# Kernel optimization log

Hardware: AMD Instinct MI355X
Metric: run time of the kernel (lower is better)

Reference implementation:

```python
import jax, jax.numpy as jnp
import numpy as np

TOPK = 2          # activate_experts
N_EXPERTS = 8     # n_routed_experts
ROUTER_SCALE = 1.0
EPS = 1e-20


def setup_inputs() -> dict:
    key = jax.random.key(0)
    ks = jax.random.split(key, 9)
    B, S, D, H, E = 4, 1024, 2048, 1792, N_EXPERTS
    w_std = 0.02  # realistic init scale so sigmoid gate is not saturated
    return {
        "x": jax.random.normal(ks[0], (B, S, D), jnp.float32),
        "gate_w": jax.random.normal(ks[1], (E, D), jnp.float32) * w_std,
        "w1_shared": jax.random.normal(ks[2], (H, D), jnp.float32) * w_std,
        "w2_shared": jax.random.normal(ks[3], (D, H), jnp.float32) * w_std,
        "w3_shared": jax.random.normal(ks[4], (H, D), jnp.float32) * w_std,
        "w1_experts": jax.random.normal(ks[5], (E, H, D), jnp.float32) * w_std,
        "w2_experts": jax.random.normal(ks[6], (E, D, H), jnp.float32) * w_std,
        "w3_experts": jax.random.normal(ks[7], (E, H, D), jnp.float32) * w_std,
        "expert_bias": jnp.zeros((E,), jnp.float32),
    }


def _swiglu(x, w1, w2, w3):
    # FeedForward.forward: w2(silu(w1(x)) * w3(x)), no biases, Identity norm
    return (jax.nn.silu(x @ w1.T) * (x @ w3.T)) @ w2.T


def reference(x, gate_w, w1_shared, w2_shared, w3_shared,
              w1_experts, w2_experts, w3_experts, expert_bias):
    B, S, D = x.shape
    xf = x.reshape(B * S, D)
    N = B * S

    # shared expert path
    out = _swiglu(xf, w1_shared, w2_shared, w3_shared)

    # ---- TokenChoiceTopKRouter ----
    scores = jax.nn.sigmoid((xf @ gate_w.T).astype(jnp.float32))      # [N, E]
    _, idx = jax.lax.top_k(scores + expert_bias[None, :], TOPK)       # [N, K]
    top = jnp.take_along_axis(scores, idx, axis=1)                    # [N, K]
    top = top / (jnp.sum(top, axis=-1, keepdims=True) + EPS)

    # dense gate matrix g[t,e] = normalized score if expert e selected for token t, else 0.
    # Equivalent to the permute -> grouped-GEMM -> scatter_add pipeline: the
    # scaling (top_scores * router_scaling_factor) is applied to the expert
    # INPUT, and since the expert FFN has no biases, FFN_e(0) == 0 for
    # unselected experts, so the scatter_add combine equals a sum over e.
    g = jnp.zeros((N, N_EXPERTS), scores.dtype)
    g = g.at[jnp.arange(N)[:, None], idx].set(top) * ROUTER_SCALE      # [N, E]

    xg = xf[:, None, :] * g[:, :, None]                                # [N, E, D]
    h = jax.nn.silu(jnp.einsum('ned,ehd->neh', xg, w1_experts)) \
        * jnp.einsum('ned,ehd->neh', xg, w3_experts)                   # [N, E, H]
    out = out + jnp.einsum('neh,edh->nd', h, w2_experts)               # combine over experts

    output = out.reshape(B, S, D)
    aux_loss = jnp.float32(0.0)  # eval mode: aux_loss = 0
    return output, aux_loss
```

## Files before the change

kernel.cpp:

```cpp
#include <hip/hip_runtime.h>
#include <stdint.h>

typedef unsigned short u16;
typedef short v8s __attribute__((ext_vector_type(8)));
typedef float v4f __attribute__((ext_vector_type(4)));

#define NTOK 4096
#define DDIM 2048
#define HDIM 1792
#define NEXP 8
#define MAXROWS 9216
#define MAXTILE 72

__device__ __forceinline__ u16 f2b(float f) {
    union { float f; uint32_t i; } v; v.f = f;
    uint32_t r = v.i + 0x7fff + ((v.i >> 16) & 1);
    return (u16)(r >> 16);
}
__device__ __forceinline__ float silu_f(float x) { return x / (1.f + __expf(-x)); }
__device__ __forceinline__ float b2f(u16 u) {
    union { float f; uint32_t i; } v; v.i = ((uint32_t)u) << 16; return v.f;
}

#define AS1 __attribute__((address_space(1)))
#define AS3 __attribute__((address_space(3)))
__device__ __forceinline__ void gload_lds16(const u16* g, u16* l) {
    __builtin_amdgcn_global_load_lds((const AS1 void*)g, (AS3 void*)l, 16, 0, 0);
}

__global__ void cvt_kernel(const float* __restrict__ in, u16* __restrict__ out, int n) {
    int i = (blockIdx.x * blockDim.x + threadIdx.x) * 4;
    if (i >= n) return;
    float4 v = *(const float4*)(in + i);
    ushort4 o;
    o.x = f2b(v.x); o.y = f2b(v.y); o.z = f2b(v.z); o.w = f2b(v.w);
    *(ushort4*)(out + i) = o;
}

__global__ void router_kernel(const float* __restrict__ x, const float* __restrict__ gw,
                              const float* __restrict__ bias,
                              int* __restrict__ topk_idx, float* __restrict__ topk_wt,
                              int* __restrict__ cnt) {
    int wave = threadIdx.x >> 6, lane = threadIdx.x & 63;
    int t = blockIdx.x * 4 + wave;
    float acc[NEXP];
#pragma unroll
    for (int e = 0; e < NEXP; e++) acc[e] = 0.f;
    const float* xr = x + (size_t)t * DDIM;
    for (int i = 0; i < DDIM / 64; i++) {
        int d = i * 64 + lane;
        float xv = xr[d];
#pragma unroll
        for (int e = 0; e < NEXP; e++) acc[e] += xv * gw[e * DDIM + d];
    }
#pragma unroll
    for (int off = 32; off > 0; off >>= 1)
#pragma unroll
        for (int e = 0; e < NEXP; e++) acc[e] += __shfl_xor(acc[e], off, 64);
    if (lane == 0) {
        float s[NEXP], sb[NEXP];
#pragma unroll
        for (int e = 0; e < NEXP; e++) {
            s[e] = 1.f / (1.f + __expf(-acc[e]));
            sb[e] = s[e] + bias[e];
        }
        int i0 = 0;
#pragma unroll
        for (int e = 1; e < NEXP; e++) if (sb[e] > sb[i0]) i0 = e;
        int i1 = -1;
#pragma unroll
        for (int e = 0; e < NEXP; e++) {
            if (e == i0) continue;
            if (i1 < 0 || sb[e] > sb[i1]) i1 = e;
        }
        float w0 = s[i0], w1 = s[i1];
        float inv = 1.f / (w0 + w1 + 1e-20f);
        topk_idx[t * 2] = i0; topk_idx[t * 2 + 1] = i1;
        topk_wt[t * 2] = w0 * inv; topk_wt[t * 2 + 1] = w1 * inv;
        atomicAdd(&cnt[i0], 1); atomicAdd(&cnt[i1], 1);
    }
}

__global__ void zero_small(int* cnt, int* cnt2) {
    if (threadIdx.x < NEXP) { cnt[threadIdx.x] = 0; cnt2[threadIdx.x] = 0; }
}

__global__ void setup_kernel(const int* __restrict__ cnt, int* __restrict__ base,
                             int* __restrict__ exp_tile, int* __restrict__ tok_of,
                             float* __restrict__ wt_of) {
    if (threadIdx.x == 0) {
        int b = 0, sb[NEXP + 1];
        for (int e = 0; e < NEXP; e++) { sb[e] = b; base[e] = b; b += (cnt[e] + 127) & ~127; }
        sb[NEXP] = b; base[NEXP] = b;
        int ntile = b >> 7;
        for (int td = 0; td < MAXTILE; td++) {
            int e = -1;
            if (td < ntile) {
                int r = td << 7;
                for (int q = 0; q < NEXP; q++)
                    if (r >= sb[q] && r < sb[q + 1]) e = q;
            }
            exp_tile[td] = e;
        }
    }
    __syncthreads();
    for (int i = threadIdx.x; i < MAXROWS; i += blockDim.x) { tok_of[i] = 0; wt_of[i] = 0.f; }
}

__global__ void assign_kernel(const int* __restrict__ topk_idx, const float* __restrict__ topk_wt,
                              const int* __restrict__ base, int* __restrict__ cnt2,
                              int* __restrict__ tok_of, float* __restrict__ wt_of) {
    int g = blockIdx.x * blockDim.x + threadIdx.x;
    int t = g >> 1, k = g & 1;
    int e = topk_idx[t * 2 + k];
    int p = base[e] + atomicAdd(&cnt2[e], 1);
    tok_of[p] = t; wt_of[p] = topk_wt[t * 2 + k];
}

template <int EPI, bool GATHER, bool EXPB, bool BF32>
__global__ __launch_bounds__(256, 2)
void gemm_nt(const u16* __restrict__ A, const void* __restrict__ Bw,
             void* __restrict__ Cout, int N, int K,
             const int* __restrict__ tok_of, const int* __restrict__ exp_tile,
             long bstride) {
    int nt = blockIdx.x, mt = blockIdx.y;
    size_t boff = 0;
    if (EXPB) {
        int e = exp_tile[mt];
        if (e < 0) return;
        boff = (size_t)e * bstride;
    }
    int m0 = mt * 128, n0 = nt * 128;
    __shared__ u16 As[128 * 64];
    __shared__ u16 Bs[128 * 64];
    int tid = threadIdx.x, lane = tid & 63, wave = tid >> 6;
    int wm = wave >> 1, wn = wave & 1;
    int quad = lane >> 4, lr = lane & 15;

    v4f acc[4][4];
#pragma unroll
    for (int i = 0; i < 4; i++)
#pragma unroll
        for (int j = 0; j < 4; j++) acc[i][j] = (v4f){0.f, 0.f, 0.f, 0.f};

    const u16* gA[4];
    const u16* gB[4];
    const float* fB[4];
    u16* sB[4];
    u16* lA[4];
    u16* lB[4];
#pragma unroll
    for (int j = 0; j < 4; j++) {
        int idx = j * 256 + tid;
        int row = idx >> 3, s = idx & 7, cc = s ^ (row & 7);
        int arow = GATHER ? tok_of[m0 + row] : (m0 + row);
        gA[j] = A + (size_t)arow * K + cc * 8;
        if (!BF32) {
            gB[j] = (const u16*)Bw + boff + (size_t)(n0 + row) * K + cc * 8;
            fB[j] = nullptr; sB[j] = nullptr;
        } else {
            gB[j] = nullptr;
            fB[j] = (const float*)Bw + boff + (size_t)(n0 + row) * K + cc * 8;
            sB[j] = Bs + (size_t)idx * 8;
        }
        int cb = (j * 256 + wave * 64) * 8;
        lA[j] = As + cb;
        lB[j] = Bs + cb;
    }

    for (int k0 = 0; k0 < K; k0 += 64) {
#pragma unroll
        for (int j = 0; j < 4; j++) gload_lds16(gA[j] + k0, lA[j]);
        if (!BF32) {
#pragma unroll
            for (int j = 0; j < 4; j++) gload_lds16(gB[j] + k0, lB[j]);
        } else {
#pragma unroll
            for (int j = 0; j < 4; j++) {
                const float* bp = fB[j] + k0;
                float4 f0 = *(const float4*)bp;
                float4 f1 = *(const float4*)(bp + 4);
                union { v8s v; u16 s[8]; } u;
                u.s[0] = f2b(f0.x); u.s[1] = f2b(f0.y); u.s[2] = f2b(f0.z); u.s[3] = f2b(f0.w);
                u.s[4] = f2b(f1.x); u.s[5] = f2b(f1.y); u.s[6] = f2b(f1.z); u.s[7] = f2b(f1.w);
                *(v8s*)sB[j] = u.v;
            }
        }
        __syncthreads();
#pragma unroll
        for (int kk = 0; kk < 64; kk += 32) {
            v8s af[4], bfr[4];
#pragma unroll
            for (int mi = 0; mi < 4; mi++) {
                int row = wm * 64 + mi * 16 + lr;
                int c = (kk >> 3) + quad;
                af[mi] = *(const v8s*)(As + row * 64 + ((c ^ (row & 7)) << 3));
            }
#pragma unroll
            for (int ni = 0; ni < 4; ni++) {
                int row = wn * 64 + ni * 16 + lr;
                int c = (kk >> 3) + quad;
                bfr[ni] = *(const v8s*)(Bs + row * 64 + ((c ^ (row & 7)) << 3));
            }
#pragma unroll
            for (int mi = 0; mi < 4; mi++)
#pragma unroll
                for (int ni = 0; ni < 4; ni++)
                    acc[mi][ni] = __builtin_amdgcn_mfma_f32_16x16x32_bf16(af[mi], bfr[ni], acc[mi][ni], 0, 0, 0);
        }
        __syncthreads();
    }

#pragma unroll
    for (int mi = 0; mi < 4; mi++)
#pragma unroll
        for (int ni = 0; ni < 4; ni++)
#pragma unroll
            for (int r = 0; r < 4; r++) {
                int gr = m0 + wm * 64 + mi * 16 + quad * 4 + r;
                int gc = n0 + wn * 64 + ni * 16 + lr;
                float v = acc[mi][ni][r];
                if (EPI == 0) {
                    ((u16*)Cout)[(size_t)gr * N + gc] = f2b(v);
                } else if (EPI == 1) {
                    ((float*)Cout)[(size_t)gr * N + gc] = v;
                } else {
                    int tok = tok_of[gr];
                    atomicAdd(&((float*)Cout)[(size_t)tok * N + gc], v);
                }
            }
}

__global__ void swiglu_kernel(u16* __restrict__ u1, const u16* __restrict__ u3,
                              const float* __restrict__ wt_of) {
    int row = blockIdx.x;
    float w = wt_of ? wt_of[row] : 1.f;
    size_t i = (size_t)row * HDIM + threadIdx.x * 4;
    ushort4 a = *(const ushort4*)(u1 + i);
    ushort4 b = *(const ushort4*)(u3 + i);
    ushort4 o;
    o.x = f2b(silu_f(w * b2f(a.x)) * (w * b2f(b.x)));
    o.y = f2b(silu_f(w * b2f(a.y)) * (w * b2f(b.y)));
    o.z = f2b(silu_f(w * b2f(a.z)) * (w * b2f(b.z)));
    o.w = f2b(silu_f(w * b2f(a.w)) * (w * b2f(b.w)));
    *(ushort4*)(u1 + i) = o;
}

__global__ void aux_kernel(float* __restrict__ out) {
    if (threadIdx.x == 0) out[(size_t)NTOK * DDIM] = 0.f;
}

extern "C" void kernel_launch(void* const* d_in, const int* in_sizes, int n_in,
                              void* d_out, int out_size, void* d_ws, size_t ws_size,
                              hipStream_t stream) {
    const float* x   = (const float*)d_in[0];
    const float* gw  = (const float*)d_in[1];
    const float* w1s = (const float*)d_in[2];
    const float* w2s = (const float*)d_in[3];
    const float* w3s = (const float*)d_in[4];
    const float* w1e = (const float*)d_in[5];
    const float* w2e = (const float*)d_in[6];
    const float* w3e = (const float*)d_in[7];
    const float* ebias = (const float*)d_in[8];
    float* outp = (float*)d_out;

    char* ws = (char*)d_ws;
    size_t off = 0;
    auto alloc = [&](size_t bytes) {
        void* p = ws + off;
        off = (off + bytes + 255) & ~(size_t)255;
        return p;
    };
    u16* xb     = (u16*)alloc((size_t)NTOK * DDIM * 2);
    u16* u1     = (u16*)alloc((size_t)MAXROWS * HDIM * 2);
    u16* u3     = (u16*)alloc((size_t)MAXROWS * HDIM * 2);
    int* topk_idx = (int*)alloc(NTOK * 2 * 4);
    float* topk_wt = (float*)alloc(NTOK * 2 * 4);
    int* cnt    = (int*)alloc(64);
    int* cnt2   = (int*)alloc(64);
    int* base   = (int*)alloc(64);
    int* exp_tile = (int*)alloc(MAXTILE * 4);
    int* tok_of = (int*)alloc(MAXROWS * 4);
    float* wt_of = (float*)alloc(MAXROWS * 4);
    const int SH = HDIM * DDIM;
    const long EX = (long)NEXP * HDIM * DDIM;
    u16* w1sb = (u16*)alloc((size_t)SH * 2);
    u16* w2sb = (u16*)alloc((size_t)SH * 2);
    u16* w3sb = (u16*)alloc((size_t)SH * 2);
    u16* w1eb = (u16*)alloc((size_t)EX * 2);
    u16* w2eb = (u16*)alloc((size_t)EX * 2);
    u16* w3eb = (u16*)alloc((size_t)EX * 2);
    bool full = (off <= ws_size);
    (void)in_sizes; (void)n_in; (void)out_size;

    zero_small<<<1, 64, 0, stream>>>(cnt, cnt2);
    router_kernel<<<NTOK / 4, 256, 0, stream>>>(x, gw, ebias, topk_idx, topk_wt, cnt);
    setup_kernel<<<1, 256, 0, stream>>>(cnt, base, exp_tile, tok_of, wt_of);
    assign_kernel<<<NTOK * 2 / 256, 256, 0, stream>>>(topk_idx, topk_wt, base, cnt2, tok_of, wt_of);

    cvt_kernel<<<(NTOK * DDIM / 4 + 255) / 256, 256, 0, stream>>>(x, xb, NTOK * DDIM);
    if (full) {
        cvt_kernel<<<(SH / 4 + 255) / 256, 256, 0, stream>>>(w1s, w1sb, SH);
        cvt_kernel<<<(SH / 4 + 255) / 256, 256, 0, stream>>>(w2s, w2sb, SH);
        cvt_kernel<<<(SH / 4 + 255) / 256, 256, 0, stream>>>(w3s, w3sb, SH);
        cvt_kernel<<<((int)(EX / 4) + 255) / 256, 256, 0, stream>>>(w1e, w1eb, (int)EX);
        cvt_kernel<<<((int)(EX / 4) + 255) / 256, 256, 0, stream>>>(w2e, w2eb, (int)EX);
        cvt_kernel<<<((int)(EX / 4) + 255) / 256, 256, 0, stream>>>(w3e, w3eb, (int)EX);
    }

    if (full) {
        gemm_nt<0, false, false, false><<<dim3(HDIM / 128, NTOK / 128), 256, 0, stream>>>(
            xb, w1sb, u1, HDIM, DDIM, nullptr, nullptr, 0);
        gemm_nt<0, false, false, false><<<dim3(HDIM / 128, NTOK / 128), 256, 0, stream>>>(
            xb, w3sb, u3, HDIM, DDIM, nullptr, nullptr, 0);
        swiglu_kernel<<<NTOK, 448, 0, stream>>>(u1, u3, nullptr);
        gemm_nt<1, false, false, false><<<dim3(DDIM / 128, NTOK / 128), 256, 0, stream>>>(
            u1, w2sb, outp, DDIM, HDIM, nullptr, nullptr, 0);
        gemm_nt<0, true, true, false><<<dim3(HDIM / 128, MAXTILE), 256, 0, stream>>>(
            xb, w1eb, u1, HDIM, DDIM, tok_of, exp_tile, (long)HDIM * DDIM);
        gemm_nt<0, true, true, false><<<dim3(HDIM / 128, MAXTILE), 256, 0, stream>>>(
            xb, w3eb, u3, HDIM, DDIM, tok_of, exp_tile, (long)HDIM * DDIM);
        swiglu_kernel<<<MAXROWS, 448, 0, stream>>>(u1, u3, wt_of);
        gemm_nt<2, false, true, false><<<dim3(DDIM / 128, MAXTILE), 256, 0, stream>>>(
            u1, w2eb, outp, DDIM, HDIM, tok_of, exp_tile, (long)DDIM * HDIM);
    } else {
        gemm_nt<0, false, false, true><<<dim3(HDIM / 128, NTOK / 128), 256, 0, stream>>>(
            xb, w1s, u1, HDIM, DDIM, nullptr, nullptr, 0);
        gemm_nt<0, false, false, true><<<dim3(HDIM / 128, NTOK / 128), 256, 0, stream>>>(
            xb, w3s, u3, HDIM, DDIM, nullptr, nullptr, 0);
        swiglu_kernel<<<NTOK, 448, 0, stream>>>(u1, u3, nullptr);
        gemm_nt<1, false, false, true><<<dim3(DDIM / 128, NTOK / 128), 256, 0, stream>>>(
            u1, w2s, outp, DDIM, HDIM, nullptr, nullptr, 0);
        gemm_nt<0, true, true, true><<<dim3(HDIM / 128, MAXTILE), 256, 0, stream>>>(
            xb, w1e, u1, HDIM, DDIM, tok_of, exp_tile, (long)HDIM * DDIM);
        gemm_nt<0, true, true, true><<<dim3(HDIM / 128, MAXTILE), 256, 0, stream>>>(
            xb, w3e, u3, HDIM, DDIM, tok_of, exp_tile, (long)HDIM * DDIM);
        swiglu_kernel<<<MAXROWS, 448, 0, stream>>>(u1, u3, wt_of);
        gemm_nt<2, false, true, true><<<dim3(DDIM / 128, MAXTILE), 256, 0, stream>>>(
            u1, w2e, outp, DDIM, HDIM, tok_of, exp_tile, (long)DDIM * HDIM);
    }

    aux_kernel<<<1, 64, 0, stream>>>(outp);
}
```

Measured before the change: 1.021 ms.

## Fold shared expert into grouped GEMM with 256x256 multi-stage pipelined tiles

The shared expert is treated as a ninth expert occupying the first 4096 rows of the grouped buffer, which removes the separate shared-path GEMM launches. The bf16 GEMM is replaced with a 256x256-tile, 512-thread kernel that keeps a 4-stage LDS ring filled by async global-to-LDS loads, uses explicit vmcnt waits and raises wave priority around the MFMA block. Per-expert padding grows to 256 rows, so more padded rows are computed. The shared output now goes through atomic adds into a zeroed output buffer, which adds a memset and extra atomic traffic.

New measurement: 1.153 ms. +13.0%, slower.

```diff
diff --git a/kernel.cpp b/kernel.cpp
--- a/kernel.cpp
+++ b/kernel.cpp
@@ -9,8 +9,10 @@
 #define DDIM 2048
 #define HDIM 1792
 #define NEXP 8
-#define MAXROWS 9216
-#define MAXTILE 72
+#define SHROWS 4096
+#define MAXROWS 14336
+#define MAXT256 56
+#define MAXT128 112
 
 __device__ __forceinline__ u16 f2b(float f) {
     union { float f; uint32_t i; } v; v.f = f;
@@ -27,6 +29,7 @@
 __device__ __forceinline__ void gload_lds16(const u16* g, u16* l) {
     __builtin_amdgcn_global_load_lds((const AS1 void*)g, (AS3 void*)l, 16, 0, 0);
 }
+#define WAITV(n) asm volatile("s_waitcnt vmcnt(" #n ")" ::: "memory")
 
 __global__ void cvt_kernel(const float* __restrict__ in, u16* __restrict__ out, int n) {
     int i = (blockIdx.x * blockDim.x + threadIdx.x) * 4;
@@ -86,25 +89,32 @@
 }
 
 __global__ void setup_kernel(const int* __restrict__ cnt, int* __restrict__ base,
-                             int* __restrict__ exp_tile, int* __restrict__ tok_of,
-                             float* __restrict__ wt_of) {
+                             int* __restrict__ exp_tile256, int* __restrict__ exp_tile128,
+                             int* __restrict__ tok_of, float* __restrict__ wt_of) {
     if (threadIdx.x == 0) {
-        int b = 0, sb[NEXP + 1];
-        for (int e = 0; e < NEXP; e++) { sb[e] = b; base[e] = b; b += (cnt[e] + 127) & ~127; }
-        sb[NEXP] = b; base[NEXP] = b;
-        int ntile = b >> 7;
-        for (int td = 0; td < MAXTILE; td++) {
-            int e = -1;
-            if (td < ntile) {
-                int r = td << 7;
-                for (int q = 0; q < NEXP; q++)
-                    if (r >= sb[q] && r < sb[q + 1]) e = q;
-            }
-            exp_tile[td] = e;
+        int b = SHROWS, sb[NEXP + 1];
+        for (int e = 0; e < NEXP; e++) { sb[e] = b; base[e] = b; b += (cnt[e] + 255) & ~255; }
+        sb[NEXP] = b;
+        for (int td = 0; td < MAXT256; td++) {
+            int e = -1, r = td << 8;
+            if (r < SHROWS) e = NEXP;
+            else for (int q = 0; q < NEXP; q++)
+                if (r >= sb[q] && r < sb[q + 1]) e = q;
+            exp_tile256[td] = e;
+        }
+        for (int td = 0; td < MAXT128; td++) {
+            int e = -1, r = td << 7;
+            if (r < SHROWS) e = NEXP;
+            else for (int q = 0; q < NEXP; q++)
+                if (r >= sb[q] && r < sb[q + 1]) e = q;
+            exp_tile128[td] = e;
         }
     }
     __syncthreads();
-    for (int i = threadIdx.x; i < MAXROWS; i += blockDim.x) { tok_of[i] = 0; wt_of[i] = 0.f; }
+    for (int i = threadIdx.x; i < MAXROWS; i += blockDim.x) {
+        tok_of[i] = (i < SHROWS) ? i : 0;
+        wt_of[i]  = (i < SHROWS) ? 1.f : 0.f;
+    }
 }
 
 __global__ void assign_kernel(const int* __restrict__ topk_idx, const float* __restrict__ topk_wt,
@@ -117,19 +127,121 @@
     tok_of[p] = t; wt_of[p] = topk_wt[t * 2 + k];
 }
 
-template <int EPI, bool GATHER, bool EXPB, bool BF32>
-__global__ __launch_bounds__(256, 2)
-void gemm_nt(const u16* __restrict__ A, const void* __restrict__ Bw,
-             void* __restrict__ Cout, int N, int K,
+template <int EPI, bool GATHER, int K>
+__global__ __launch_bounds__(512, 2)
+void gemm256(const u16* __restrict__ A, const u16* __restrict__ Bw,
+             void* __restrict__ Cout, int N,
              const int* __restrict__ tok_of, const int* __restrict__ exp_tile,
              long bstride) {
+    constexpr int NT = K / 32;
     int nt = blockIdx.x, mt = blockIdx.y;
-    size_t boff = 0;
-    if (EXPB) {
-        int e = exp_tile[mt];
-        if (e < 0) return;
-        boff = (size_t)e * bstride;
-    }
+    int e = exp_tile[mt];
+    if (e < 0) return;
+    const u16* Bp = Bw + (size_t)e * bstride;
+    int m0 = mt * 256, n0 = nt * 256;
+
+    __shared__ u16 smem[4 * 2 * 8192];
+    int tid = threadIdx.x, lane = tid & 63, wave = tid >> 6;
+    int wm = wave >> 2, wn = wave & 3, quad = lane >> 4, lr = lane & 15;
+
+    v4f acc[8][4];
+#pragma unroll
+    for (int i = 0; i < 8; i++)
+#pragma unroll
+        for (int j = 0; j < 4; j++) acc[i][j] = (v4f){0.f, 0.f, 0.f, 0.f};
+
+    const u16* gA[2]; const u16* gB[2]; int ldso[2];
+#pragma unroll
+    for (int j = 0; j < 2; j++) {
+        int idx = j * 512 + tid;
+        int R = idx >> 3, s = idx & 7, cc = s ^ (R & 7);
+        int r = (R << 1) | (cc >> 2);
+        int col = (cc & 3) * 8;
+        int ar = GATHER ? tok_of[m0 + r] : (m0 + r);
+        gA[j] = A + (size_t)ar * K + col;
+        gB[j] = Bp + (size_t)(n0 + r) * K + col;
+        ldso[j] = (j * 512 + wave * 64) * 8;
+    }
+    int offA[8], offB[4];
+#pragma unroll
+    for (int mi = 0; mi < 8; mi++) {
+        int r = wm * 128 + mi * 16 + lr;
+        int R = r >> 1, cc = ((r & 1) << 2) | quad;
+        offA[mi] = R * 64 + ((cc ^ (R & 7)) << 3);
+    }
+#pragma unroll
+    for (int ni = 0; ni < 4; ni++) {
+        int r = wn * 64 + ni * 16 + lr;
+        int R = r >> 1, cc = ((r & 1) << 2) | quad;
+        offB[ni] = R * 64 + ((cc ^ (R & 7)) << 3);
+    }
+
+    auto STAGE = [&](int t) {
+        u16* base = smem + (t & 3) * 16384;
+        int k0 = t * 32;
+#pragma unroll
+        for (int j = 0; j < 2; j++) gload_lds16(gA[j] + k0, base + ldso[j]);
+#pragma unroll
+        for (int j = 0; j < 2; j++) gload_lds16(gB[j] + k0, base + 8192 + ldso[j]);
+    };
+
+    STAGE(0); STAGE(1); STAGE(2);
+
+#pragma unroll 1
+    for (int t = 0; t < NT; t++) {
+        if (t + 3 < NT) STAGE(t + 3);
+        if      (t + 3 < NT) { WAITV(12); }
+        else if (t + 2 < NT) { WAITV(8); }
+        else if (t + 1 < NT) { WAITV(4); }
+        else                 { WAITV(0); }
+        __builtin_amdgcn_s_barrier();
+        const u16* sa = smem + (t & 3) * 16384;
+        const u16* sb = sa + 8192;
+        v8s af[8], bfr[4];
+#pragma unroll
+        for (int mi = 0; mi < 8; mi++) af[mi] = *(const v8s*)(sa + offA[mi]);
+#pragma unroll
+        for (int ni = 0; ni < 4; ni++) bfr[ni] = *(const v8s*)(sb + offB[ni]);
+        asm volatile("s_waitcnt lgkmcnt(0)" ::: "memory");
+        __builtin_amdgcn_sched_barrier(0);
+        __builtin_amdgcn_s_setprio(1);
+#pragma unroll
+        for (int mi = 0; mi < 8; mi++)
+#pragma unroll
+            for (int ni = 0; ni < 4; ni++)
+                acc[mi][ni] = __builtin_amdgcn_mfma_f32_16x16x32_bf16(af[mi], bfr[ni], acc[mi][ni], 0, 0, 0);
+        __builtin_amdgcn_s_setprio(0);
+        __builtin_amdgcn_s_barrier();
+    }
+
+#pragma unroll
+    for (int mi = 0; mi < 8; mi++)
+#pragma unroll
+        for (int ni = 0; ni < 4; ni++)
+#pragma unroll
+            for (int r = 0; r < 4; r++) {
+                int gr = m0 + wm * 128 + mi * 16 + quad * 4 + r;
+                int gc = n0 + wn * 64 + ni * 16 + lr;
+                float v = acc[mi][ni][r];
+                if (EPI == 0) {
+                    ((u16*)Cout)[(size_t)gr * N + gc] = f2b(v);
+                } else {
+                    int tok = tok_of[gr];
+                    atomicAdd(&((float*)Cout)[(size_t)tok * N + gc], v);
+                }
+            }
+}
+
+template <int EPI, bool GATHER>
+__global__ __launch_bounds__(256, 2)
+void gemm_nt_f32(const u16* __restrict__ A, const float* __restrict__ Bw,
+                 const float* __restrict__ Bsh, void* __restrict__ Cout, int N, int K,
+                 const int* __restrict__ tok_of, const int* __restrict__ exp_tile,
+                 long bstride) {
+    int nt = blockIdx.x, mt = blockIdx.y;
+    int e = exp_tile[mt];
+    if (e < 0) return;
+    const float* Bp = (e == NEXP) ? Bsh : (Bw + (size_t)e * bstride);
     int m0 = mt * 128, n0 = nt * 128;
     __shared__ u16 As[128 * 64];
     __shared__ u16 Bs[128 * 64];
@@ -143,48 +255,30 @@
 #pragma unroll
         for (int j = 0; j < 4; j++) acc[i][j] = (v4f){0.f, 0.f, 0.f, 0.f};
 
-    const u16* gA[4];
-    const u16* gB[4];
-    const float* fB[4];
-    u16* sB[4];
-    u16* lA[4];
-    u16* lB[4];
+    const u16* gA[4]; const float* fB[4]; u16* sB[4]; u16* lA[4];
 #pragma unroll
     for (int j = 0; j < 4; j++) {
         int idx = j * 256 + tid;
         int row = idx >> 3, s = idx & 7, cc = s ^ (row & 7);
         int arow = GATHER ? tok_of[m0 + row] : (m0 + row);
         gA[j] = A + (size_t)arow * K + cc * 8;
-        if (!BF32) {
-            gB[j] = (const u16*)Bw + boff + (size_t)(n0 + row) * K + cc * 8;
-            fB[j] = nullptr; sB[j] = nullptr;
-        } else {
-            gB[j] = nullptr;
-            fB[j] = (const float*)Bw + boff + (size_t)(n0 + row) * K + cc * 8;
-            sB[j] = Bs + (size_t)idx * 8;
-        }
-        int cb = (j * 256 + wave * 64) * 8;
-        lA[j] = As + cb;
-        lB[j] = Bs + cb;
+        fB[j] = Bp + (size_t)(n0 + row) * K + cc * 8;
+        sB[j] = Bs + (size_t)idx * 8;
+        lA[j] = As + (j * 256 + wave * 64) * 8;
     }
 
     for (int k0 = 0; k0 < K; k0 += 64) {
 #pragma unroll
         for (int j = 0; j < 4; j++) gload_lds16(gA[j] + k0, lA[j]);
-        if (!BF32) {
-#pragma unroll
-            for (int j = 0; j < 4; j++) gload_lds16(gB[j] + k0, lB[j]);
-        } else {
-#pragma unroll
-            for (int j = 0; j < 4; j++) {
-                const float* bp = fB[j] + k0;
-                float4 f0 = *(const float4*)bp;
-                float4 f1 = *(const float4*)(bp + 4);
-                union { v8s v; u16 s[8]; } u;
-                u.s[0] = f2b(f0.x); u.s[1] = f2b(f0.y); u.s[2] = f2b(f0.z); u.s[3] = f2b(f0.w);
-                u.s[4] = f2b(f1.x); u.s[5] = f2b(f1.y); u.s[6] = f2b(f1.z); u.s[7] = f2b(f1.w);
-                *(v8s*)sB[j] = u.v;
-            }
+#pragma unroll
+        for (int j = 0; j < 4; j++) {
+            const float* bp = fB[j] + k0;
+            float4 f0 = *(const float4*)bp;
+            float4 f1 = *(const float4*)(bp + 4);
+            union { v8s v; u16 s[8]; } u;
+            u.s[0] = f2b(f0.x); u.s[1] = f2b(f0.y); u.s[2] = f2b(f0.z); u.s[3] = f2b(f0.w);
+            u.s[4] = f2b(f1.x); u.s[5] = f2b(f1.y); u.s[6] = f2b(f1.z); u.s[7] = f2b(f1.w);
+            *(v8s*)sB[j] = u.v;
         }
         __syncthreads();
 #pragma unroll
@@ -222,8 +316,6 @@
                 float v = acc[mi][ni][r];
                 if (EPI == 0) {
                     ((u16*)Cout)[(size_t)gr * N + gc] = f2b(v);
-                } else if (EPI == 1) {
-                    ((float*)Cout)[(size_t)gr * N + gc] = v;
                 } else {
                     int tok = tok_of[gr];
                     atomicAdd(&((float*)Cout)[(size_t)tok * N + gc], v);
@@ -234,7 +326,7 @@
 __global__ void swiglu_kernel(u16* __restrict__ u1, const u16* __restrict__ u3,
                               const float* __restrict__ wt_of) {
     int row = blockIdx.x;
-    float w = wt_of ? wt_of[row] : 1.f;
+    float w = wt_of[row];
     size_t i = (size_t)row * HDIM + threadIdx.x * 4;
     ushort4 a = *(const ushort4*)(u1 + i);
     ushort4 b = *(const ushort4*)(u3 + i);
@@ -279,65 +371,48 @@
     int* cnt    = (int*)alloc(64);
     int* cnt2   = (int*)alloc(64);
     int* base   = (int*)alloc(64);
-    int* exp_tile = (int*)alloc(MAXTILE * 4);
+    int* exp_tile256 = (int*)alloc(MAXT256 * 4);
+    int* exp_tile128 = (int*)alloc(MAXT128 * 4);
     int* tok_of = (int*)alloc(MAXROWS * 4);
     float* wt_of = (float*)alloc(MAXROWS * 4);
     const int SH = HDIM * DDIM;
-    const long EX = (long)NEXP * HDIM * DDIM;
-    u16* w1sb = (u16*)alloc((size_t)SH * 2);
-    u16* w2sb = (u16*)alloc((size_t)SH * 2);
-    u16* w3sb = (u16*)alloc((size_t)SH * 2);
-    u16* w1eb = (u16*)alloc((size_t)EX * 2);
-    u16* w2eb = (u16*)alloc((size_t)EX * 2);
-    u16* w3eb = (u16*)alloc((size_t)EX * 2);
+    const int EX8 = 8 * SH;
+    u16* w1eb = (u16*)alloc((size_t)9 * SH * 2);
+    u16* w2eb = (u16*)alloc((size_t)9 * SH * 2);
+    u16* w3eb = (u16*)alloc((size_t)9 * SH * 2);
     bool full = (off <= ws_size);
     (void)in_sizes; (void)n_in; (void)out_size;
 
+    hipMemsetAsync(outp, 0, (size_t)NTOK * DDIM * sizeof(float), stream);
     zero_small<<<1, 64, 0, stream>>>(cnt, cnt2);
     router_kernel<<<NTOK / 4, 256, 0, stream>>>(x, gw, ebias, topk_idx, topk_wt, cnt);
-    setup_kernel<<<1, 256, 0, stream>>>(cnt, base, exp_tile, tok_of, wt_of);
+    setup_kernel<<<1, 256, 0, stream>>>(cnt, base, exp_tile256, exp_tile128, tok_of, wt_of);
     assign_kernel<<<NTOK * 2 / 256, 256, 0, stream>>>(topk_idx, topk_wt, base, cnt2, tok_of, wt_of);
 
     cvt_kernel<<<(NTOK * DDIM / 4 + 255) / 256, 256, 0, stream>>>(x, xb, NTOK * DDIM);
     if (full) {
-        cvt_kernel<<<(SH / 4 + 255) / 256, 256, 0, stream>>>(w1s, w1sb, SH);
-        cvt_kernel<<<(SH / 4 + 255) / 256, 256, 0, stream>>>(w2s, w2sb, SH);
-        cvt_kernel<<<(SH / 4 + 255) / 256, 256, 0, stream>>>(w3s, w3sb, SH);
-        cvt_kernel<<<((int)(EX / 4) + 255) / 256, 256, 0, stream>>>(w1e, w1eb, (int)EX);
-        cvt_kernel<<<((int)(EX / 4) + 255) / 256, 256, 0, stream>>>(w2e, w2eb, (int)EX);
-        cvt_kernel<<<((int)(EX / 4) + 255) / 256, 256, 0, stream>>>(w3e, w3eb, (int)EX);
-    }
-
-    if (full) {
-        gemm_nt<0, false, false, false><<<dim3(HDIM / 128, NTOK / 128), 256, 0, stream>>>(
-            xb, w1sb, u1, HDIM, DDIM, nullptr, nullptr, 0);
-        gemm_nt<0, false, false, false><<<dim3(HDIM / 128, NTOK / 128), 256, 0, stream>>>(
-            xb, w3sb, u3, HDIM, DDIM, nullptr, nullptr, 0);
-        swiglu_kernel<<<NTOK, 448, 0, stream>>>(u1, u3, nullptr);
-        gemm_nt<1, false, false, false><<<dim3(DDIM / 128, NTOK / 128), 256, 0, stream>>>(
-            u1, w2sb, outp, DDIM, HDIM, nullptr, nullptr, 0);
-        gemm_nt<0, true, true, false><<<dim3(HDIM / 128, MAXTILE), 256, 0, stream>>>(
-            xb, w1eb, u1, HDIM, DDIM, tok_of, exp_tile, (long)HDIM * DDIM);
-        gemm_nt<0, true, true, false><<<dim3(HDIM / 128, MAXTILE), 256, 0, stream>>>(
-            xb, w3eb, u3, HDIM, DDIM, tok_of, exp_tile, (long)HDIM * DDIM);
+        cvt_kernel<<<(EX8 / 4 + 255) / 256, 256, 0, stream>>>(w1e, w1eb, EX8);
+        cvt_kernel<<<(SH / 4 + 255) / 256, 256, 0, stream>>>(w1s, w1eb + (size_t)8 * SH, SH);
+        cvt_kernel<<<(EX8 / 4 + 255) / 256, 256, 0, stream>>>(w2e, w2eb, EX8);
+        cvt_kernel<<<(SH / 4 + 255) / 256, 256, 0, stream>>>(w2s, w2eb + (size_t)8 * SH, SH);
+        cvt_kernel<<<(EX8 / 4 + 255) / 256, 256, 0, stream>>>(w3e, w3eb, EX8);
+        cvt_kernel<<<(SH / 4 + 255) / 256, 256, 0, stream>>>(w3s, w3eb + (size_t)8 * SH, SH);
+
+        gemm256<0, true, DDIM><<<dim3(HDIM / 256, MAXT256), 512, 0, stream>>>(
+            xb, w1eb, u1, HDIM, tok_of, exp_tile256, (long)SH);
+        gemm256<0, true, DDIM><<<dim3(HDIM / 256, MAXT256), 512, 0, stream>>>(
+            xb, w3eb, u3, HDIM, tok_of, exp_tile256, (long)SH);
         swiglu_kernel<<<MAXROWS, 448, 0, stream>>>(u1, u3, wt_of);
-        gemm_nt<2, false, true, false><<<dim3(DDIM / 128, MAXTILE), 256, 0, stream>>>(
-            u1, w2eb, outp, DDIM, HDIM, tok_of, exp_tile, (long)DDIM * HDIM);
+        gemm256<2, false, HDIM><<<dim3(DDIM / 256, MAXT256), 512, 0, stream>>>(
+            u1, w2eb, outp, DDIM, tok_of, exp_tile256, (long)SH);
     } else {
-        gemm_nt<0, false, false, true><<<dim3(HDIM / 128, NTOK / 128), 256, 0, stream>>>(
-            xb, w1s, u1, HDIM, DDIM, nullptr, nullptr, 0);
-        gemm_nt<0, false, false, true><<<dim3(HDIM / 128, NTOK / 128), 256, 0, stream>>>(
-            xb, w3s, u3, HDIM, DDIM, nullptr, nullptr, 0);
-        swiglu_kernel<<<NTOK, 448, 0, stream>>>(u1, u3, nullptr);
-        gemm_nt<1, false, false, true><<<dim3(DDIM / 128, NTOK / 128), 256, 0, stream>>>(
-            u1, w2s, outp, DDIM, HDIM, nullptr, nullptr, 0);
-        gemm_nt<0, true, true, true><<<dim3(HDIM / 128, MAXTILE), 256, 0, stream>>>(
-            xb, w1e, u1, HDIM, DDIM, tok_of, exp_tile, (long)HDIM * DDIM);
-        gemm_nt<0, true, true, true><<<dim3(HDIM / 128, MAXTILE), 256, 0, stream>>>(
-            xb, w3e, u3, HDIM, DDIM, tok_of, exp_tile, (long)HDIM * DDIM);
+        gemm_nt_f32<0, true><<<dim3(HDIM / 128, MAXT128), 256, 0, stream>>>(
+            xb, w1e, w1s, u1, HDIM, DDIM, tok_of, exp_tile128, (long)SH);
+        gemm_nt_f32<0, true><<<dim3(HDIM / 128, MAXT128), 256, 0, stream>>>(
+            xb, w3e, w3s, u3, HDIM, DDIM, tok_of, exp_tile128, (long)SH);
         swiglu_kernel<<<MAXROWS, 448, 0, stream>>>(u1, u3, wt_of);
-        gemm_nt<2, false, true, true><<<dim3(DDIM / 128, MAXTILE), 256, 0, stream>>>(
-            u1, w2e, outp, DDIM, HDIM, tok_of, exp_tile, (long)DDIM * HDIM);
+        gemm_nt_f32<2, false><<<dim3(DDIM / 128, MAXT128), 256, 0, stream>>>(
+            u1, w2e, w2s, outp, DDIM, HDIM, tok_of, exp_tile128, (long)SH);
     }
 
     aux_kernel<<<1, 64, 0, stream>>>(outp);
```
